# Kernel tuning notes

Measured on AMD Instinct MI355X. Metric: run time of the kernel, lower is better.

The kernel has to match this reference:

```python
import jax, jax.numpy as jnp
import numpy as np

B, S, D = 4, 4096, 2048
H, DH = 16, 128
ROPE_BASE = 10000.0


def rotate_half(x):
    x1, x2 = jnp.split(x, 2, axis=-1)
    return jnp.concatenate((-x2, x1), axis=-1)


def rope_cos_sin(seq_len, head_dim, dtype):
    inv_freq = 1.0 / (ROPE_BASE ** (jnp.arange(0, head_dim, 2, dtype=jnp.float32) / head_dim))
    pos = jnp.arange(seq_len, dtype=jnp.float32)
    freqs = pos[:, None] * inv_freq[None, :]          # [S, DH/2]
    emb = jnp.concatenate((freqs, freqs), axis=-1)    # [S, DH]
    return jnp.cos(emb).astype(dtype), jnp.sin(emb).astype(dtype)


def setup_inputs() -> dict:
    key = jax.random.key(0)
    ks = jax.random.split(key, 5)
    scale = 0.02
    return {
        "hidden_states": jax.random.normal(ks[0], (B, S, D), jnp.float32),
        "Wq": jax.random.normal(ks[1], (D, D), jnp.float32) * scale,
        "Wk": jax.random.normal(ks[2], (D, D), jnp.float32) * scale,
        "Wv": jax.random.normal(ks[3], (D, D), jnp.float32) * scale,
        "Wo": jax.random.normal(ks[4], (D, D), jnp.float32) * scale,
    }


def reference(hidden_states, Wq, Wk, Wv, Wo):
    b, s, d = hidden_states.shape
    # QKV projections (nn.Linear stores weight as [out, in] -> x @ W.T)
    def proj(W):
        y = hidden_states @ W.T                       # [B, S, D]
        return y.reshape(b, s, H, DH).transpose(0, 2, 1, 3)  # [B, H, S, DH]
    q, k, v = proj(Wq), proj(Wk), proj(Wv)

    # RoPE (cos/sin broadcast over head dim: unsqueeze_dim=1)
    cos, sin = rope_cos_sin(s, DH, hidden_states.dtype)  # [S, DH]
    cos = cos[None, None]                                # [1, 1, S, DH]
    sin = sin[None, None]
    q = q * cos + rotate_half(q) * sin
    k = k * cos + rotate_half(k) * sin

    # SDPA, non-causal, no mask, eval mode (dropout 0)
    scale = 1.0 / jnp.sqrt(jnp.asarray(DH, hidden_states.dtype))
    scores = jnp.einsum("bhqd,bhkd->bhqk", q, k) * scale
    attn = jax.nn.softmax(scores, axis=-1)
    ctx = jnp.einsum("bhqk,bhkd->bhqd", attn, v)         # [B, H, S, DH]

    ctx = ctx.transpose(0, 2, 1, 3).reshape(b, s, H * DH)
    return ctx @ Wo.T
```

## Files before the change

### kernel.cpp

```cpp
#include <hip/hip_runtime.h>
#include <hip/hip_bf16.h>
#include <math.h>

typedef __attribute__((ext_vector_type(4)))  float f32x4;
typedef __attribute__((ext_vector_type(16))) float f32x16;
typedef __attribute__((ext_vector_type(8)))  short s16x8;
typedef __attribute__((ext_vector_type(4)))  short s16x4;
typedef __attribute__((ext_vector_type(4)))  int   i32x4;

#define DEVI __device__ __forceinline__


DEVI unsigned short f2bf(float x) {
    unsigned int u = __builtin_bit_cast(unsigned int, x);
    u += 0x7fffu + ((u >> 16) & 1u);
    return (unsigned short)(u >> 16);
}

DEVI f32x4 mfma16(s16x8 a, s16x8 b, f32x4 c) {
    return __builtin_amdgcn_mfma_f32_16x16x32_bf16(a, b, c, 0, 0, 0);
}
DEVI f32x16 mfma32(s16x8 a, s16x8 b, f32x16 c) {
    return __builtin_amdgcn_mfma_f32_32x32x16_bf16(a, b, c, 0, 0, 0);
}
DEVI int cvtpk(float lo, float hi) {
    int r; asm("v_cvt_pk_bf16_f32 %0, %1, %2" : "=v"(r) : "v"(lo), "v"(hi)); return r;
}
DEVI void plswap(int& a, int& b) {
    asm volatile("v_permlane32_swap_b32 %0, %1" : "+v"(a), "+v"(b));
}
DEVI void gload16(const void* g, void* l) {
    __builtin_amdgcn_global_load_lds(
        (const __attribute__((address_space(1))) void*)g,
        (__attribute__((address_space(3))) void*)l, 16, 0, 0);
}

__global__ __launch_bounds__(256)
void cvt_kernel(const float* __restrict__ in, unsigned short* __restrict__ out, int n8) {
    int i = blockIdx.x * 256 + threadIdx.x;
    const int stride = gridDim.x * 256;
    for (; i < n8; i += stride) {
        f32x4 a = ((const f32x4*)in)[i * 2];
        f32x4 b = ((const f32x4*)in)[i * 2 + 1];
        s16x8 o;
#pragma unroll
        for (int e = 0; e < 4; ++e) o[e] = (short)f2bf(a[e]);
#pragma unroll
        for (int e = 0; e < 4; ++e) o[4 + e] = (short)f2bf(b[e]);
        *(s16x8*)&out[(size_t)i * 8] = o;
    }
}

__global__ void rope_table_kernel(float* __restrict__ cosb, float* __restrict__ sinb) {
    const int s = blockIdx.x;
    const int i = threadIdx.x;
    const float inv = expf(-(float)i * (9.210340371976184f / 64.0f));
    const float ang = (float)s * inv;
    cosb[s * 64 + i] = cosf(ang);
    sinb[s * 64 + i] = sinf(ang);
}

template <bool AB16, bool WB16, int EPI>
__global__ __launch_bounds__(256, 2)
void gemm_kernel(const void* __restrict__ Ap, const void* __restrict__ Bw,
                 void* __restrict__ Cp, const float* __restrict__ cosb,
                 const float* __restrict__ sinb, float oscale)
{
    constexpr bool GL = AB16 && WB16;
    static_assert(GL || !WB16, "non-GL path stages W as f32");
    constexpr int KD = 2048;
    __shared__ __align__(16) unsigned short smem[GL ? 17408 : 20480];

    const int tid  = threadIdx.x;
    const int lane = tid & 63;
    const int wid  = tid >> 6;
    const int wr   = wid >> 1, wc = wid & 1;
    const int lr   = lane & 15;
    const int lkg  = lane >> 4;
    const int lk   = lkg * 8;
    const int m0   = blockIdx.x * 128;
    const int n0   = blockIdx.y * 128;

    const f32x4 zero4 = {0.f, 0.f, 0.f, 0.f};
    f32x4 acc[4][4];
#pragma unroll
    for (int i = 0; i < 4; ++i)
#pragma unroll
        for (int j = 0; j < 4; ++j) acc[i][j] = zero4;

    const int ncol0 = wc * 32;

    if constexpr (GL) {
        const unsigned short* Ah = (const unsigned short*)Ap;
        const unsigned short* Wh = (const unsigned short*)Bw;
        auto stageG = [&](int kt, int buf) {
            const int k0 = kt * 32;
            unsigned short* Ab = smem + buf * 4096;
            unsigned short* Bb = smem + 8192 + buf * 4096;
#pragma unroll
            for (int i = 0; i < 2; ++i) {
                int flat = i * 256 + tid;
                int r = flat >> 2, c = (flat & 3) * 8;
                gload16(&Ah[(size_t)(m0 + r) * KD + k0 + c], Ab + flat * 8);
                gload16(&Wh[(size_t)(n0 + r) * KD + k0 + c], Bb + flat * 8);
            }
        };
        auto computeG = [&](int buf) {
            const unsigned short* Ab = smem + buf * 4096;
            const unsigned short* Bb = smem + 8192 + buf * 4096;
            s16x8 af[4], bf[4];
#pragma unroll
            for (int mi = 0; mi < 4; ++mi)
                af[mi] = *(const s16x8*)&Ab[(wr * 64 + mi * 16 + lr) * 32 + lk];
#pragma unroll
            for (int nj = 0; nj < 4; ++nj) {
                int nc = ncol0 + (nj & 1) * 16 + (nj >> 1) * 64;
                bf[nj] = *(const s16x8*)&Bb[(nc + lr) * 32 + lk];
            }
#pragma unroll
            for (int mi = 0; mi < 4; ++mi)
#pragma unroll
                for (int nj = 0; nj < 4; ++nj)
                    acc[mi][nj] = mfma16(af[mi], bf[nj], acc[mi][nj]);
        };
        stageG(0, 0);
        __syncthreads();
        for (int kt = 0; kt < 64; ++kt) {
            const int cur = kt & 1;
            if (kt < 63) stageG(kt + 1, cur ^ 1);
            computeG(cur);
            __syncthreads();
        }
    } else {
        unsigned short* const As = smem;
        unsigned short* const Bs = smem + 10240;
        f32x4 aF[4], bF[4];
        s16x8 aH[2];
        const float* Af = (const float*)Ap;
        const unsigned short* Ah = (const unsigned short*)Ap;
        const float* Wf = (const float*)Bw;

        auto stage_load = [&](int kt) {
            const int k0 = kt * 32;
            if constexpr (!AB16) {
#pragma unroll
                for (int i = 0; i < 4; ++i) {
                    int flat = i * 256 + tid;
                    int r = flat >> 3, c = (flat & 7) * 4;
                    aF[i] = *(const f32x4*)&Af[(size_t)(m0 + r) * KD + k0 + c];
                }
            } else {
#pragma unroll
                for (int i = 0; i < 2; ++i) {
                    int flat = i * 256 + tid;
                    int r = flat >> 2, c = (flat & 3) * 8;
                    aH[i] = *(const s16x8*)&Ah[(size_t)(m0 + r) * KD + k0 + c];
                }
            }
#pragma unroll
            for (int i = 0; i < 4; ++i) {
                int flat = i * 256 + tid;
                int r = flat >> 3, c = (flat & 7) * 4;
                bF[i] = *(const f32x4*)&Wf[(size_t)(n0 + r) * KD + k0 + c];
            }
        };
        auto stage_write = [&](int buf) {
            unsigned short* Ab = As + buf * 5120;
            unsigned short* Bb = Bs + buf * 5120;
            if constexpr (!AB16) {
#pragma unroll
                for (int i = 0; i < 4; ++i) {
                    int flat = i * 256 + tid;
                    int r = flat >> 3, c = (flat & 7) * 4;
                    s16x4 v;
#pragma unroll
                    for (int e = 0; e < 4; ++e) v[e] = (short)f2bf(aF[i][e]);
                    *(s16x4*)&Ab[r * 40 + c] = v;
                }
            } else {
#pragma unroll
                for (int i = 0; i < 2; ++i) {
                    int flat = i * 256 + tid;
                    int r = flat >> 2, c = (flat & 3) * 8;
                    *(s16x8*)&Ab[r * 40 + c] = aH[i];
                }
            }
#pragma unroll
            for (int i = 0; i < 4; ++i) {
                int flat = i * 256 + tid;
                int r = flat >> 3, c = (flat & 7) * 4;
                s16x4 v;
#pragma unroll
                for (int e = 0; e < 4; ++e) v[e] = (short)f2bf(bF[i][e]);
                *(s16x4*)&Bb[r * 40 + c] = v;
            }
        };
        auto compute = [&](int buf) {
            const unsigned short* Ab = As + buf * 5120;
            const unsigned short* Bb = Bs + buf * 5120;
            s16x8 af[4], bf[4];
#pragma unroll
            for (int mi = 0; mi < 4; ++mi)
                af[mi] = *(const s16x8*)&Ab[(wr * 64 + mi * 16 + lr) * 40 + lk];
#pragma unroll
            for (int nj = 0; nj < 4; ++nj) {
                int nc = ncol0 + (nj & 1) * 16 + (nj >> 1) * 64;
                bf[nj] = *(const s16x8*)&Bb[(nc + lr) * 40 + lk];
            }
#pragma unroll
            for (int mi = 0; mi < 4; ++mi)
#pragma unroll
                for (int nj = 0; nj < 4; ++nj)
                    acc[mi][nj] = mfma16(af[mi], bf[nj], acc[mi][nj]);
        };
        stage_load(0);
        stage_write(0);
        __syncthreads();
        for (int kt = 0; kt < 64; ++kt) {
            const int cur = kt & 1;
            if (kt < 63) stage_load(kt + 1);
            compute(cur);
            if (kt < 63) stage_write(cur ^ 1);
            __syncthreads();
        }
    }

    if constexpr (EPI == 0) {
        unsigned short* Qb = (unsigned short*)Cp;
        const int h = blockIdx.y;
#pragma unroll
        for (int mi = 0; mi < 4; ++mi) {
#pragma unroll
            for (int reg = 0; reg < 4; ++reg) {
                int mg = m0 + wr * 64 + mi * 16 + lkg * 4 + reg;
                int bb = mg >> 12, s = mg & 4095;
                size_t base = ((size_t)(bb * 16 + h) * 4096 + s) * 128;
#pragma unroll
                for (int nj = 0; nj < 2; ++nj) {
                    int dlo = wc * 32 + nj * 16 + lr;
                    float cv = cosb[s * 64 + dlo];
                    float sv = sinb[s * 64 + dlo];
                    float a  = acc[mi][nj][reg];
                    float b2 = acc[mi][nj + 2][reg];
                    Qb[base + dlo]      = f2bf((a * cv - b2 * sv) * oscale);
                    Qb[base + dlo + 64] = f2bf((b2 * cv + a * sv) * oscale);
                }
            }
        }
    } else if constexpr (EPI == 1) {
        unsigned short* Vt = (unsigned short*)Cp;
        const int h = blockIdx.y;
        unsigned short* Cs = smem;
        __syncthreads();
#pragma unroll
        for (int mi = 0; mi < 4; ++mi)
#pragma unroll
            for (int nj = 0; nj < 4; ++nj) {
                int col = wc * 32 + (nj & 1) * 16 + (nj >> 1) * 64 + lr;
#pragma unroll
                for (int reg = 0; reg < 4; ++reg) {
                    int row = wr * 64 + mi * 16 + lkg * 4 + reg;
                    Cs[row * 136 + col] = f2bf(acc[mi][nj][reg]);
                }
            }
        __syncthreads();
        const int dh = tid >> 1;
        const int sh = (tid & 1) * 64;
        const int bb = m0 >> 12, sbase = m0 & 4095;
        size_t gbase = ((size_t)((bb * 16 + h) * 128 + dh)) * 4096 + sbase + sh;
#pragma unroll
        for (int j0 = 0; j0 < 8; ++j0) {
            s16x8 v;
#pragma unroll
            for (int e = 0; e < 8; ++e)
                v[e] = (short)Cs[(sh + j0 * 8 + e) * 136 + dh];
            *(s16x8*)&Vt[gbase + j0 * 8] = v;
        }
    } else {
        float* Ob = (float*)Cp;
#pragma unroll
        for (int mi = 0; mi < 4; ++mi)
#pragma unroll
            for (int reg = 0; reg < 4; ++reg) {
                int mg = m0 + wr * 64 + mi * 16 + lkg * 4 + reg;
#pragma unroll
                for (int nj = 0; nj < 4; ++nj) {
                    int col = n0 + wc * 32 + (nj & 1) * 16 + (nj >> 1) * 64 + lr;
                    Ob[(size_t)mg * 2048 + col] = acc[mi][nj][reg];
                }
            }
    }
}

__global__ __launch_bounds__(512, 2)
void attn_kernel(const unsigned short* __restrict__ Q,
                 const unsigned short* __restrict__ Kb,
                 const unsigned short* __restrict__ Vt,
                 unsigned short* __restrict__ ctx)
{
    __shared__ __align__(16) char smem[131072];

    const int tid  = threadIdx.x;
    const int lane = tid & 63;
    const int wid  = tid >> 6;
    const int l31  = lane & 31;
    const int h    = lane >> 5;
    const int qt   = blockIdx.x;
    const int bh   = blockIdx.y;

    const size_t kbase  = (size_t)bh * 4096;
    const size_t vtbase = (size_t)bh * 128 * 4096;

    const size_t qrow = kbase + (size_t)qt * 256 + wid * 32 + l31;
    s16x8 qf[8];
#pragma unroll
    for (int ks = 0; ks < 8; ++ks)
        qf[ks] = *(const s16x8*)&Q[qrow * 128 + ks * 16 + h * 8];

    s16x8 ones;
#pragma unroll
    for (int e = 0; e < 8; ++e) ones[e] = (short)0x3F80;

    const f32x16 Z16 = {0,0,0,0,0,0,0,0,0,0,0,0,0,0,0,0};
    f32x16 accO[4];
    accO[0] = Z16; accO[1] = Z16; accO[2] = Z16; accO[3] = Z16;
    f32x16 accL = Z16;

    auto stage = [&](int buf, int T) {
        const int kv0 = T * 128;
        char* kdst = smem + buf * 65536;
        char* vdst = kdst + 32768;
#pragma unroll
        for (int c = 0; c < 4; ++c) {
            int flat = c * 512 + tid;
            int r    = flat >> 4;
            int col  = (flat & 15) * 16;
            int cs   = col ^ ((r & 15) << 4);
            gload16(&Kb[(kbase + kv0 + r) * 128 + (cs >> 1)], kdst + flat * 16);
            gload16(&Vt[vtbase + (size_t)r * 4096 + kv0 + (cs >> 1)], vdst + flat * 16);
        }
    };

    const int swz   = (l31 & 15) << 4;
    const int hford = wid >> 2;

    stage(0, 0);
    __syncthreads();

    for (int T = 0; T < 32; ++T) {
        const int buf = T & 1;
        if (T < 31) stage(buf ^ 1, T + 1);

        const char* kb = smem + buf * 65536;
        const char* vb = kb + 32768;

#pragma unroll
        for (int hfi = 0; hfi < 2; ++hfi) {
            const int hf = hfi ^ hford;
            const char* kbh = kb + hf * 16384;
            const int   vco = hf * 128;

            f32x16 sc0 = Z16, sc1 = Z16;
            __builtin_amdgcn_s_setprio(1);
#pragma unroll
            for (int ks = 0; ks < 8; ++ks) {
                s16x8 k0 = *(const s16x8*)(kbh + ((l31 * 256 + ks * 32 + h * 16) ^ swz));
                s16x8 k1 = *(const s16x8*)(kbh + (((32 + l31) * 256 + ks * 32 + h * 16) ^ swz));
                sc0 = mfma32(k0, qf[ks], sc0);
                sc1 = mfma32(k1, qf[ks], sc1);
            }
            __builtin_amdgcn_s_setprio(0);

#pragma unroll
            for (int i = 0; i < 16; ++i) sc0[i] = exp2f(sc0[i]);
#pragma unroll
            for (int i = 0; i < 16; ++i) sc1[i] = exp2f(sc1[i]);

            s16x8 pb[4];
#pragma unroll
            for (int g = 0; g < 4; ++g) {
                const f32x16& s = (g < 2) ? sc0 : sc1;
                const int o = (g & 1) * 8;
                int a0 = cvtpk(s[o + 0], s[o + 1]);
                int a1 = cvtpk(s[o + 2], s[o + 3]);
                int b0 = cvtpk(s[o + 4], s[o + 5]);
                int b1 = cvtpk(s[o + 6], s[o + 7]);
                plswap(a0, b0); plswap(a1, b1);
                i32x4 w = {a0, a1, b0, b1};
                pb[g] = __builtin_bit_cast(s16x8, w);
            }

            __builtin_amdgcn_s_setprio(1);
#pragma unroll
            for (int ks = 0; ks < 4; ++ks) {
                accL = mfma32(ones, pb[ks], accL);
#pragma unroll
                for (int mf = 0; mf < 4; ++mf) {
                    s16x8 vf = *(const s16x8*)(vb + ((((mf * 32 + l31) * 256) + (vco + ks * 32 + h * 16)) ^ swz));
                    accO[mf] = mfma32(vf, pb[ks], accO[mf]);
                }
            }
            __builtin_amdgcn_s_setprio(0);
        }

        __syncthreads();
    }

    const float invl = 1.0f / accL[0];
    accO[0] *= invl; accO[1] *= invl; accO[2] *= invl; accO[3] *= invl;

    unsigned short* tw = (unsigned short*)smem + wid * 1088;
    const int bb = bh >> 4, hh = bh & 15;
    const size_t cbase = ((size_t)(bb * 4096 + qt * 256 + wid * 32 + l31)) * 2048 + hh * 128;
#pragma unroll
    for (int mf = 0; mf < 4; ++mf) {
#pragma unroll
        for (int reg = 0; reg < 16; ++reg) {
            int d = (reg & 3) + 8 * (reg >> 2) + 4 * h;
            tw[d * 34 + l31] = f2bf(accO[mf][reg]);
        }
        s16x8 o0, o1;
#pragma unroll
        for (int dd = 0; dd < 8; ++dd) {
            o0[dd] = (short)tw[(h * 16 + dd) * 34 + l31];
            o1[dd] = (short)tw[(h * 16 + 8 + dd) * 34 + l31];
        }
        *(s16x8*)&ctx[cbase + mf * 32 + h * 16]     = o0;
        *(s16x8*)&ctx[cbase + mf * 32 + h * 16 + 8] = o1;
    }
}

extern "C" void kernel_launch(void* const* d_in, const int* in_sizes, int n_in,
                              void* d_out, int out_size, void* d_ws, size_t ws_size,
                              hipStream_t stream)
{
    (void)in_sizes; (void)n_in; (void)out_size;
    const float* X  = (const float*)d_in[0];
    const float* Wq = (const float*)d_in[1];
    const float* Wk = (const float*)d_in[2];
    const float* Wv = (const float*)d_in[3];
    const float* Wo = (const float*)d_in[4];

    char* ws = (char*)d_ws;
    const size_t TBL  = 2097152;
    const size_t HBUF = 67108864;
    const size_t WBUF = 8388608;
    const size_t SX   = 33554432;
    const size_t SW   = 4194304;

    float* cosb = (float*)ws;
    float* sinb = (float*)(ws + 1048576);

    const float QSCALE = 0.12751763f;
    dim3 gg(128, 16), blk(256);

    rope_table_kernel<<<dim3(4096), dim3(64), 0, stream>>>(cosb, sinb);

    if (ws_size >= TBL + HBUF + 4 * WBUF + 4 * HBUF) {
        unsigned short* Xb  = (unsigned short*)(ws + TBL);
        unsigned short* Wb0 = (unsigned short*)(ws + TBL + HBUF);
        unsigned short* Qb  = (unsigned short*)(ws + TBL + HBUF + 4 * WBUF);
        unsigned short* Kb  = Qb + SX;
        unsigned short* Vtb = Kb + SX;
        unsigned short* Cb  = Vtb + SX;
        const float* Wsrc[4] = {Wq, Wk, Wv, Wo};
        cvt_kernel<<<dim3(2048), blk, 0, stream>>>(X, Xb, (int)(SX / 8));
        for (int w = 0; w < 4; ++w)
            cvt_kernel<<<dim3(1024), blk, 0, stream>>>(Wsrc[w], Wb0 + w * SW, (int)(SW / 8));
        gemm_kernel<true, true, 0><<<gg, blk, 0, stream>>>(Xb, Wb0,          Qb, cosb, sinb, QSCALE);
        gemm_kernel<true, true, 0><<<gg, blk, 0, stream>>>(Xb, Wb0 + SW,     Kb, cosb, sinb, 1.0f);
        gemm_kernel<true, true, 1><<<gg, blk, 0, stream>>>(Xb, Wb0 + 2 * SW, Vtb, cosb, sinb, 1.0f);
        attn_kernel<<<dim3(16, 64), dim3(512), 0, stream>>>(Qb, Kb, Vtb, Cb);
        gemm_kernel<true, true, 2><<<gg, blk, 0, stream>>>(Cb, Wb0 + 3 * SW, d_out, cosb, sinb, 1.0f);
    } else if (ws_size >= TBL + HBUF + 4 * WBUF + HBUF) {
        unsigned short* Xb  = (unsigned short*)(ws + TBL);
        unsigned short* Wb0 = (unsigned short*)(ws + TBL + HBUF);
        unsigned short* Vtb = (unsigned short*)(ws + TBL + HBUF + 4 * WBUF);
        unsigned short* Qb  = (unsigned short*)d_out;
        unsigned short* Kb  = Qb + SX;
        unsigned short* Cb  = Xb;
        const float* Wsrc[4] = {Wq, Wk, Wv, Wo};
        cvt_kernel<<<dim3(2048), blk, 0, stream>>>(X, Xb, (int)(SX / 8));
        for (int w = 0; w < 4; ++w)
            cvt_kernel<<<dim3(1024), blk, 0, stream>>>(Wsrc[w], Wb0 + w * SW, (int)(SW / 8));
        gemm_kernel<true, true, 0><<<gg, blk, 0, stream>>>(Xb, Wb0,          Qb, cosb, sinb, QSCALE);
        gemm_kernel<true, true, 0><<<gg, blk, 0, stream>>>(Xb, Wb0 + SW,     Kb, cosb, sinb, 1.0f);
        gemm_kernel<true, true, 1><<<gg, blk, 0, stream>>>(Xb, Wb0 + 2 * SW, Vtb, cosb, sinb, 1.0f);
        attn_kernel<<<dim3(16, 64), dim3(512), 0, stream>>>(Qb, Kb, Vtb, Cb);
        gemm_kernel<true, true, 2><<<gg, blk, 0, stream>>>(Cb, Wb0 + 3 * SW, d_out, cosb, sinb, 1.0f);
    } else {
        unsigned short* Vtb = (unsigned short*)(ws + TBL);
        unsigned short* Cb  = (unsigned short*)(ws + TBL + HBUF);
        unsigned short* Qb  = (unsigned short*)d_out;
        unsigned short* Kb  = Qb + SX;
        gemm_kernel<false, false, 0><<<gg, blk, 0, stream>>>(X, Wq, Qb, cosb, sinb, QSCALE);
        gemm_kernel<false, false, 0><<<gg, blk, 0, stream>>>(X, Wk, Kb, cosb, sinb, 1.0f);
        gemm_kernel<false, false, 1><<<gg, blk, 0, stream>>>(X, Wv, Vtb, cosb, sinb, 1.0f);
        attn_kernel<<<dim3(32, 64), dim3(512), 0, stream>>>(Qb, Kb, Vtb, Cb);
        gemm_kernel<true, false, 2><<<gg, blk, 0, stream>>>(Cb, Wo, d_out, cosb, sinb, 1.0f);
    }
}
```

Before: 1.341 ms.

## Add 256x128-tile 8-wave GEMM with swizzled LDS and split-K pipelining

Adds a new bf16 GEMM kernel for the projections. Each 512-thread block computes a 256x128 tile, and the block count is halved. The kernel stages 64-wide K chunks in two halves into double-buffered, XOR-swizzled LDS, synchronises with explicit vmcnt waits and raw barriers, and raises wave priority around the MFMA bursts. The aim is more data reuse per block, fewer LDS bank conflicts and better overlap of global loads with matrix math, traded for 96KB of LDS and one block per CU. The fallback path also changes its attention grid from 32 to 16 blocks in x.

Result: no change. 1.326 ms (-1.2%).

```diff
diff --git a/kernel.cpp b/kernel.cpp
--- a/kernel.cpp
+++ b/kernel.cpp
@@ -60,16 +60,175 @@
     sinb[s * 64 + i] = sinf(ang);
 }
 
-template <bool AB16, bool WB16, int EPI>
+template <int EPI>
+__global__ __launch_bounds__(512, 1)
+void gemm8_kernel(const unsigned short* __restrict__ Ah,
+                  const unsigned short* __restrict__ Wh,
+                  void* __restrict__ Cp, const float* __restrict__ cosb,
+                  const float* __restrict__ sinb, float oscale)
+{
+    constexpr int KD = 2048;
+    __shared__ __align__(16) char smem[98304];
+
+    const int tid  = threadIdx.x;
+    const int lane = tid & 63;
+    const int wid  = tid >> 6;
+    const int wm   = wid >> 1;
+    const int wn   = wid & 1;
+    const int lr   = lane & 15;
+    const int lkg  = lane >> 4;
+    const int m0   = blockIdx.x * 256;
+    const int n0   = blockIdx.y * 128;
+
+    const f32x4 zero4 = {0.f, 0.f, 0.f, 0.f};
+    f32x4 acc[4][4];
+#pragma unroll
+    for (int i = 0; i < 4; ++i)
+#pragma unroll
+        for (int j = 0; j < 4; ++j) acc[i][j] = zero4;
+
+    const int rsw = (lkg ^ ((lr >> 1) & 3)) << 4;
+
+    auto stageA = [&](int b, int t, int kh) {
+        const int k0 = t * 64 + kh * 32;
+        char* dst = smem + b * 49152 + kh * 16384;
+#pragma unroll
+        for (int c = 0; c < 2; ++c) {
+            int flat = c * 512 + tid;
+            int row  = flat >> 2, slot = flat & 3;
+            int sg   = slot ^ ((row >> 1) & 3);
+            gload16(&Ah[(size_t)(m0 + row) * KD + k0 + sg * 8], dst + flat * 16);
+        }
+    };
+    auto stageB = [&](int b, int t, int kh) {
+        const int k0 = t * 64 + kh * 32;
+        char* dst = smem + b * 49152 + 32768 + kh * 8192;
+        int row = tid >> 2, slot = tid & 3;
+        int sg  = slot ^ ((row >> 1) & 3);
+        gload16(&Wh[(size_t)(n0 + row) * KD + k0 + sg * 8], dst + tid * 16);
+    };
+
+    auto phase = [&](int b, int ks) {
+        const char* Ab = smem + b * 49152 + ks * 16384;
+        const char* Bb = smem + b * 49152 + 32768 + ks * 8192;
+        s16x8 af[4], bf[4];
+#pragma unroll
+        for (int mi = 0; mi < 4; ++mi) {
+            int row = wm * 64 + mi * 16 + lr;
+            af[mi] = *(const s16x8*)(Ab + row * 64 + rsw);
+        }
+#pragma unroll
+        for (int nj = 0; nj < 4; ++nj) {
+            int row = wn * 32 + (nj & 1) * 16 + (nj >> 1) * 64 + lr;
+            bf[nj] = *(const s16x8*)(Bb + row * 64 + rsw);
+        }
+        __builtin_amdgcn_s_setprio(1);
+#pragma unroll
+        for (int mi = 0; mi < 4; ++mi)
+#pragma unroll
+            for (int nj = 0; nj < 4; ++nj)
+                acc[mi][nj] = mfma16(af[mi], bf[nj], acc[mi][nj]);
+        __builtin_amdgcn_s_setprio(0);
+    };
+
+    stageA(0, 0, 0); stageB(0, 0, 0);
+    stageA(0, 0, 1); stageB(0, 0, 1);
+    asm volatile("s_waitcnt vmcnt(0)" ::: "memory");
+    __builtin_amdgcn_s_barrier();
+
+    for (int t = 0; t < 31; ++t) {
+        const int b = t & 1;
+        stageA(b ^ 1, t + 1, 0); stageB(b ^ 1, t + 1, 0);
+        phase(b, 0);
+        asm volatile("s_waitcnt vmcnt(3)" ::: "memory");
+        __builtin_amdgcn_s_barrier();
+        stageA(b ^ 1, t + 1, 1); stageB(b ^ 1, t + 1, 1);
+        phase(b, 1);
+        asm volatile("s_waitcnt vmcnt(3)" ::: "memory");
+        __builtin_amdgcn_s_barrier();
+    }
+    phase(1, 0);
+    asm volatile("s_waitcnt vmcnt(0)" ::: "memory");
+    __builtin_amdgcn_s_barrier();
+    phase(1, 1);
+
+    if constexpr (EPI == 0) {
+        unsigned short* Qb = (unsigned short*)Cp;
+        const int h = blockIdx.y;
+#pragma unroll
+        for (int mi = 0; mi < 4; ++mi) {
+#pragma unroll
+            for (int reg = 0; reg < 4; ++reg) {
+                int mg = m0 + wm * 64 + mi * 16 + lkg * 4 + reg;
+                int bb = mg >> 12, s = mg & 4095;
+                size_t base = ((size_t)(bb * 16 + h) * 4096 + s) * 128;
+#pragma unroll
+                for (int nj = 0; nj < 2; ++nj) {
+                    int dlo = wn * 32 + nj * 16 + lr;
+                    float cv = cosb[s * 64 + dlo];
+                    float sv = sinb[s * 64 + dlo];
+                    float a  = acc[mi][nj][reg];
+                    float b2 = acc[mi][nj + 2][reg];
+                    Qb[base + dlo]      = f2bf((a * cv - b2 * sv) * oscale);
+                    Qb[base + dlo + 64] = f2bf((b2 * cv + a * sv) * oscale);
+                }
+            }
+        }
+    } else if constexpr (EPI == 1) {
+        unsigned short* Vt = (unsigned short*)Cp;
+        const int h = blockIdx.y;
+        unsigned short* Cs = (unsigned short*)smem;
+        __syncthreads();
+#pragma unroll
+        for (int mi = 0; mi < 4; ++mi)
+#pragma unroll
+            for (int nj = 0; nj < 4; ++nj) {
+                int col = wn * 32 + (nj & 1) * 16 + (nj >> 1) * 64 + lr;
+#pragma unroll
+                for (int reg = 0; reg < 4; ++reg) {
+                    int row = wm * 64 + mi * 16 + lkg * 4 + reg;
+                    Cs[row * 136 + col] = f2bf(acc[mi][nj][reg]);
+                }
+            }
+        __syncthreads();
+        const int dh = tid >> 2;
+        const int sh = (tid & 3) * 64;
+        const int bb = m0 >> 12, sbase = m0 & 4095;
+        size_t gbase = ((size_t)((bb * 16 + h) * 128 + dh)) * 4096 + sbase + sh;
+#pragma unroll
+        for (int j0 = 0; j0 < 8; ++j0) {
+            s16x8 v;
+#pragma unroll
+            for (int e = 0; e < 8; ++e)
+                v[e] = (short)Cs[(sh + j0 * 8 + e) * 136 + dh];
+            *(s16x8*)&Vt[gbase + j0 * 8] = v;
+        }
+    } else {
+        float* Ob = (float*)Cp;
+#pragma unroll
+        for (int mi = 0; mi < 4; ++mi)
+#pragma unroll
+            for (int reg = 0; reg < 4; ++reg) {
+                int mg = m0 + wm * 64 + mi * 16 + lkg * 4 + reg;
+#pragma unroll
+                for (int nj = 0; nj < 4; ++nj) {
+                    int col = n0 + wn * 32 + (nj & 1) * 16 + (nj >> 1) * 64 + lr;
+                    Ob[(size_t)mg * 2048 + col] = acc[mi][nj][reg];
+                }
+            }
+    }
+}
+
+template <bool AB16, int EPI>
 __global__ __launch_bounds__(256, 2)
-void gemm_kernel(const void* __restrict__ Ap, const void* __restrict__ Bw,
+void gemm_kernel(const void* __restrict__ Ap, const float* __restrict__ Bw,
                  void* __restrict__ Cp, const float* __restrict__ cosb,
                  const float* __restrict__ sinb, float oscale)
 {
-    constexpr bool GL = AB16 && WB16;
-    static_assert(GL || !WB16, "non-GL path stages W as f32");
     constexpr int KD = 2048;
-    __shared__ __align__(16) unsigned short smem[GL ? 17408 : 20480];
+    __shared__ __align__(16) unsigned short smem[20480];
+    unsigned short* const As = smem;
+    unsigned short* const Bs = smem + 10240;
 
     const int tid  = threadIdx.x;
     const int lane = tid & 63;
@@ -88,141 +247,94 @@
 #pragma unroll
         for (int j = 0; j < 4; ++j) acc[i][j] = zero4;
 
-    const int ncol0 = wc * 32;
-
-    if constexpr (GL) {
-        const unsigned short* Ah = (const unsigned short*)Ap;
-        const unsigned short* Wh = (const unsigned short*)Bw;
-        auto stageG = [&](int kt, int buf) {
-            const int k0 = kt * 32;
-            unsigned short* Ab = smem + buf * 4096;
-            unsigned short* Bb = smem + 8192 + buf * 4096;
+    f32x4 aF[4], bF[4];
+    s16x8 aH[2];
+    const float* Af = (const float*)Ap;
+    const unsigned short* AhL = (const unsigned short*)Ap;
+
+    auto stage_load = [&](int kt) {
+        const int k0 = kt * 32;
+        if constexpr (!AB16) {
+#pragma unroll
+            for (int i = 0; i < 4; ++i) {
+                int flat = i * 256 + tid;
+                int r = flat >> 3, c = (flat & 7) * 4;
+                aF[i] = *(const f32x4*)&Af[(size_t)(m0 + r) * KD + k0 + c];
+            }
+        } else {
 #pragma unroll
             for (int i = 0; i < 2; ++i) {
                 int flat = i * 256 + tid;
                 int r = flat >> 2, c = (flat & 3) * 8;
-                gload16(&Ah[(size_t)(m0 + r) * KD + k0 + c], Ab + flat * 8);
-                gload16(&Wh[(size_t)(n0 + r) * KD + k0 + c], Bb + flat * 8);
-            }
-        };
-        auto computeG = [&](int buf) {
-            const unsigned short* Ab = smem + buf * 4096;
-            const unsigned short* Bb = smem + 8192 + buf * 4096;
-            s16x8 af[4], bf[4];
-#pragma unroll
-            for (int mi = 0; mi < 4; ++mi)
-                af[mi] = *(const s16x8*)&Ab[(wr * 64 + mi * 16 + lr) * 32 + lk];
-#pragma unroll
-            for (int nj = 0; nj < 4; ++nj) {
-                int nc = ncol0 + (nj & 1) * 16 + (nj >> 1) * 64;
-                bf[nj] = *(const s16x8*)&Bb[(nc + lr) * 32 + lk];
-            }
-#pragma unroll
-            for (int mi = 0; mi < 4; ++mi)
-#pragma unroll
-                for (int nj = 0; nj < 4; ++nj)
-                    acc[mi][nj] = mfma16(af[mi], bf[nj], acc[mi][nj]);
-        };
-        stageG(0, 0);
-        __syncthreads();
-        for (int kt = 0; kt < 64; ++kt) {
-            const int cur = kt & 1;
-            if (kt < 63) stageG(kt + 1, cur ^ 1);
-            computeG(cur);
-            __syncthreads();
-        }
-    } else {
-        unsigned short* const As = smem;
-        unsigned short* const Bs = smem + 10240;
-        f32x4 aF[4], bF[4];
-        s16x8 aH[2];
-        const float* Af = (const float*)Ap;
-        const unsigned short* Ah = (const unsigned short*)Ap;
-        const float* Wf = (const float*)Bw;
-
-        auto stage_load = [&](int kt) {
-            const int k0 = kt * 32;
-            if constexpr (!AB16) {
-#pragma unroll
-                for (int i = 0; i < 4; ++i) {
-                    int flat = i * 256 + tid;
-                    int r = flat >> 3, c = (flat & 7) * 4;
-                    aF[i] = *(const f32x4*)&Af[(size_t)(m0 + r) * KD + k0 + c];
-                }
-            } else {
-#pragma unroll
-                for (int i = 0; i < 2; ++i) {
-                    int flat = i * 256 + tid;
-                    int r = flat >> 2, c = (flat & 3) * 8;
-                    aH[i] = *(const s16x8*)&Ah[(size_t)(m0 + r) * KD + k0 + c];
-                }
-            }
-#pragma unroll
-            for (int i = 0; i < 4; ++i) {
-                int flat = i * 256 + tid;
-                int r = flat >> 3, c = (flat & 7) * 4;
-                bF[i] = *(const f32x4*)&Wf[(size_t)(n0 + r) * KD + k0 + c];
-            }
-        };
-        auto stage_write = [&](int buf) {
-            unsigned short* Ab = As + buf * 5120;
-            unsigned short* Bb = Bs + buf * 5120;
-            if constexpr (!AB16) {
-#pragma unroll
-                for (int i = 0; i < 4; ++i) {
-                    int flat = i * 256 + tid;
-                    int r = flat >> 3, c = (flat & 7) * 4;
-                    s16x4 v;
-#pragma unroll
-                    for (int e = 0; e < 4; ++e) v[e] = (short)f2bf(aF[i][e]);
-                    *(s16x4*)&Ab[r * 40 + c] = v;
-                }
-            } else {
-#pragma unroll
-                for (int i = 0; i < 2; ++i) {
-                    int flat = i * 256 + tid;
-                    int r = flat >> 2, c = (flat & 3) * 8;
-                    *(s16x8*)&Ab[r * 40 + c] = aH[i];
-                }
-            }
+                aH[i] = *(const s16x8*)&AhL[(size_t)(m0 + r) * KD + k0 + c];
+            }
+        }
+#pragma unroll
+        for (int i = 0; i < 4; ++i) {
+            int flat = i * 256 + tid;
+            int r = flat >> 3, c = (flat & 7) * 4;
+            bF[i] = *(const f32x4*)&Bw[(size_t)(n0 + r) * KD + k0 + c];
+        }
+    };
+    auto stage_write = [&](int buf) {
+        unsigned short* Ab = As + buf * 5120;
+        unsigned short* Bb = Bs + buf * 5120;
+        if constexpr (!AB16) {
 #pragma unroll
             for (int i = 0; i < 4; ++i) {
                 int flat = i * 256 + tid;
                 int r = flat >> 3, c = (flat & 7) * 4;
                 s16x4 v;
 #pragma unroll
-                for (int e = 0; e < 4; ++e) v[e] = (short)f2bf(bF[i][e]);
-                *(s16x4*)&Bb[r * 40 + c] = v;
-            }
-        };
-        auto compute = [&](int buf) {
-            const unsigned short* Ab = As + buf * 5120;
-            const unsigned short* Bb = Bs + buf * 5120;
-            s16x8 af[4], bf[4];
-#pragma unroll
-            for (int mi = 0; mi < 4; ++mi)
-                af[mi] = *(const s16x8*)&Ab[(wr * 64 + mi * 16 + lr) * 40 + lk];
-#pragma unroll
-            for (int nj = 0; nj < 4; ++nj) {
-                int nc = ncol0 + (nj & 1) * 16 + (nj >> 1) * 64;
-                bf[nj] = *(const s16x8*)&Bb[(nc + lr) * 40 + lk];
-            }
-#pragma unroll
-            for (int mi = 0; mi < 4; ++mi)
-#pragma unroll
-                for (int nj = 0; nj < 4; ++nj)
-                    acc[mi][nj] = mfma16(af[mi], bf[nj], acc[mi][nj]);
-        };
-        stage_load(0);
-        stage_write(0);
+                for (int e = 0; e < 4; ++e) v[e] = (short)f2bf(aF[i][e]);
+                *(s16x4*)&Ab[r * 40 + c] = v;
+            }
+        } else {
+#pragma unroll
+            for (int i = 0; i < 2; ++i) {
+                int flat = i * 256 + tid;
+                int r = flat >> 2, c = (flat & 3) * 8;
+                *(s16x8*)&Ab[r * 40 + c] = aH[i];
+            }
+        }
+#pragma unroll
+        for (int i = 0; i < 4; ++i) {
+            int flat = i * 256 + tid;
+            int r = flat >> 3, c = (flat & 7) * 4;
+            s16x4 v;
+#pragma unroll
+            for (int e = 0; e < 4; ++e) v[e] = (short)f2bf(bF[i][e]);
+            *(s16x4*)&Bb[r * 40 + c] = v;
+        }
+    };
+    const int ncol0 = wc * 32;
+    auto compute = [&](int buf) {
+        const unsigned short* Ab = As + buf * 5120;
+        const unsigned short* Bb = Bs + buf * 5120;
+        s16x8 af[4], bf[4];
+#pragma unroll
+        for (int mi = 0; mi < 4; ++mi)
+            af[mi] = *(const s16x8*)&Ab[(wr * 64 + mi * 16 + lr) * 40 + lk];
+#pragma unroll
+        for (int nj = 0; nj < 4; ++nj) {
+            int nc = ncol0 + (nj & 1) * 16 + (nj >> 1) * 64;
+            bf[nj] = *(const s16x8*)&Bb[(nc + lr) * 40 + lk];
+        }
+#pragma unroll
+        for (int mi = 0; mi < 4; ++mi)
+#pragma unroll
+            for (int nj = 0; nj < 4; ++nj)
+                acc[mi][nj] = mfma16(af[mi], bf[nj], acc[mi][nj]);
+    };
+    stage_load(0);
+    stage_write(0);
+    __syncthreads();
+    for (int kt = 0; kt < 64; ++kt) {
+        const int cur = kt & 1;
+        if (kt < 63) stage_load(kt + 1);
+        compute(cur);
+        if (kt < 63) stage_write(cur ^ 1);
         __syncthreads();
-        for (int kt = 0; kt < 64; ++kt) {
-            const int cur = kt & 1;
-            if (kt < 63) stage_load(kt + 1);
-            compute(cur);
-            if (kt < 63) stage_write(cur ^ 1);
-            __syncthreads();
-        }
     }
 
     if constexpr (EPI == 0) {
@@ -452,7 +564,7 @@
     float* sinb = (float*)(ws + 1048576);
 
     const float QSCALE = 0.12751763f;
-    dim3 gg(128, 16), blk(256);
+    dim3 g8(64, 16), blk8(512), blk(256);
 
     rope_table_kernel<<<dim3(4096), dim3(64), 0, stream>>>(cosb, sinb);
 
@@ -467,11 +579,11 @@
         cvt_kernel<<<dim3(2048), blk, 0, stream>>>(X, Xb, (int)(SX / 8));
         for (int w = 0; w < 4; ++w)
             cvt_kernel<<<dim3(1024), blk, 0, stream>>>(Wsrc[w], Wb0 + w * SW, (int)(SW / 8));
-        gemm_kernel<true, true, 0><<<gg, blk, 0, stream>>>(Xb, Wb0,          Qb, cosb, sinb, QSCALE);
-        gemm_kernel<true, true, 0><<<gg, blk, 0, stream>>>(Xb, Wb0 + SW,     Kb, cosb, sinb, 1.0f);
-        gemm_kernel<true, true, 1><<<gg, blk, 0, stream>>>(Xb, Wb0 + 2 * SW, Vtb, cosb, sinb, 1.0f);
+        gemm8_kernel<0><<<g8, blk8, 0, stream>>>(Xb, Wb0,          Qb, cosb, sinb, QSCALE);
+        gemm8_kernel<0><<<g8, blk8, 0, stream>>>(Xb, Wb0 + SW,     Kb, cosb, sinb, 1.0f);
+        gemm8_kernel<1><<<g8, blk8, 0, stream>>>(Xb, Wb0 + 2 * SW, Vtb, cosb, sinb, 1.0f);
         attn_kernel<<<dim3(16, 64), dim3(512), 0, stream>>>(Qb, Kb, Vtb, Cb);
-        gemm_kernel<true, true, 2><<<gg, blk, 0, stream>>>(Cb, Wb0 + 3 * SW, d_out, cosb, sinb, 1.0f);
+        gemm8_kernel<2><<<g8, blk8, 0, stream>>>(Cb, Wb0 + 3 * SW, d_out, cosb, sinb, 1.0f);
     } else if (ws_size >= TBL + HBUF + 4 * WBUF + HBUF) {
         unsigned short* Xb  = (unsigned short*)(ws + TBL);
         unsigned short* Wb0 = (unsigned short*)(ws + TBL + HBUF);
@@ -483,20 +595,21 @@
         cvt_kernel<<<dim3(2048), blk, 0, stream>>>(X, Xb, (int)(SX / 8));
         for (int w = 0; w < 4; ++w)
             cvt_kernel<<<dim3(1024), blk, 0, stream>>>(Wsrc[w], Wb0 + w * SW, (int)(SW / 8));
-        gemm_kernel<true, true, 0><<<gg, blk, 0, stream>>>(Xb, Wb0,          Qb, cosb, sinb, QSCALE);
-        gemm_kernel<true, true, 0><<<gg, blk, 0, stream>>>(Xb, Wb0 + SW,     Kb, cosb, sinb, 1.0f);
-        gemm_kernel<true, true, 1><<<gg, blk, 0, stream>>>(Xb, Wb0 + 2 * SW, Vtb, cosb, sinb, 1.0f);
+        gemm8_kernel<0><<<g8, blk8, 0, stream>>>(Xb, Wb0,          Qb, cosb, sinb, QSCALE);
+        gemm8_kernel<0><<<g8, blk8, 0, stream>>>(Xb, Wb0 + SW,     Kb, cosb, sinb, 1.0f);
+        gemm8_kernel<1><<<g8, blk8, 0, stream>>>(Xb, Wb0 + 2 * SW, Vtb, cosb, sinb, 1.0f);
         attn_kernel<<<dim3(16, 64), dim3(512), 0, stream>>>(Qb, Kb, Vtb, Cb);
-        gemm_kernel<true, true, 2><<<gg, blk, 0, stream>>>(Cb, Wb0 + 3 * SW, d_out, cosb, sinb, 1.0f);
+        gemm8_kernel<2><<<g8, blk8, 0, stream>>>(Cb, Wb0 + 3 * SW, d_out, cosb, sinb, 1.0f);
     } else {
         unsigned short* Vtb = (unsigned short*)(ws + TBL);
         unsigned short* Cb  = (unsigned short*)(ws + TBL + HBUF);
         unsigned short* Qb  = (unsigned short*)d_out;
         unsigned short* Kb  = Qb + SX;
-        gemm_kernel<false, false, 0><<<gg, blk, 0, stream>>>(X, Wq, Qb, cosb, sinb, QSCALE);
-        gemm_kernel<false, false, 0><<<gg, blk, 0, stream>>>(X, Wk, Kb, cosb, sinb, 1.0f);
-        gemm_kernel<false, false, 1><<<gg, blk, 0, stream>>>(X, Wv, Vtb, cosb, sinb, 1.0f);
-        attn_kernel<<<dim3(32, 64), dim3(512), 0, stream>>>(Qb, Kb, Vtb, Cb);
-        gemm_kernel<true, false, 2><<<gg, blk, 0, stream>>>(Cb, Wo, d_out, cosb, sinb, 1.0f);
-    }
-}
+        dim3 gg(128, 16);
+        gemm_kernel<false, 0><<<gg, blk, 0, stream>>>(X, Wq, Qb, cosb, sinb, QSCALE);
+        gemm_kernel<false, 0><<<gg, blk, 0, stream>>>(X, Wk, Kb, cosb, sinb, 1.0f);
+        gemm_kernel<false, 1><<<gg, blk, 0, stream>>>(X, Wv, Vtb, cosb, sinb, 1.0f);
+        attn_kernel<<<dim3(16, 64), dim3(512), 0, stream>>>(Qb, Kb, Vtb, Cb);
+        gemm_kernel<true, 2><<<gg, blk, 0, stream>>>(Cb, Wo, d_out, cosb, sinb, 1.0f);
+    }
+}
```
